# Optimization experiments

Measured on AMD Instinct MI355X. Metric: run time of the kernel, lower is better.

Reference implementation:

```python
import jax, jax.numpy as jnp
import numpy as np

B, Hh, Ww, D = 16, 32, 32, 1024
NH, HD = 16, 64
S = Hh * Ww


def _rotate_pairwise(x):
    # (..., d) -> pairwise rotation: (x0,x1,x2,x3,...) -> (-x1,x0,-x3,x2,...)
    x = x.reshape(*x.shape[:-1], -1, 2)
    x1, x2 = x[..., 0], x[..., 1]
    return jnp.stack((-x2, x1), axis=-1).reshape(*x.shape[:-2], -1)


def setup_inputs() -> dict:
    key = jax.random.key(0)
    ks = jax.random.split(key, 12)
    s = 1.0 / np.sqrt(D)
    return {
        "hidden_states": jax.random.normal(ks[0], (B, Hh, Ww, D), jnp.float32),
        "cos": jax.random.uniform(ks[1], (S, HD), jnp.float32, -1.0, 1.0),
        "sin": jax.random.uniform(ks[2], (S, HD), jnp.float32, -1.0, 1.0),
        "Wq": jax.random.normal(ks[3], (D, D), jnp.float32) * s,
        "bq": jnp.zeros((D,), jnp.float32),
        "Wk": jax.random.normal(ks[4], (D, D), jnp.float32) * s,
        "bk": jnp.zeros((D,), jnp.float32),
        "Wv": jax.random.normal(ks[5], (D, D), jnp.float32) * s,
        "bv": jnp.zeros((D,), jnp.float32),
        "Wo": jax.random.normal(ks[6], (D, D), jnp.float32) * s,
        "bo": jnp.zeros((D,), jnp.float32),
    }


def reference(hidden_states, cos, sin, Wq, bq, Wk, bk, Wv, bv, Wo, bo):
    b, h, w, d = hidden_states.shape
    seq = h * w
    x = hidden_states.reshape(b, seq, d)
    # QKV projections -> (b, heads, seq, head_dim)
    def proj(W, bias):
        y = x @ W.T + bias
        return y.reshape(b, seq, NH, HD).transpose(0, 2, 1, 3)
    q, k, v = proj(Wq, bq), proj(Wk, bk), proj(Wv, bv)
    # RoPE in fp32; cos/sin (seq, head_dim) broadcast over (b, heads)
    qf = q.astype(jnp.float32)
    kf = k.astype(jnp.float32)
    q = (qf * cos + _rotate_pairwise(qf) * sin).astype(q.dtype)
    k = (kf * cos + _rotate_pairwise(kf) * sin).astype(k.dtype)
    # SDPA
    scale = HD ** -0.5
    scores = jnp.einsum("bhqd,bhkd->bhqk", q, k) * scale
    attn = jax.nn.softmax(scores, axis=-1)
    out = jnp.einsum("bhqk,bhkd->bhqd", attn, v)
    out = out.transpose(0, 2, 1, 3).reshape(b, h, w, d)
    return out @ Wo.T + bo
```

## Files before the change

kernel.cpp:

```cpp
#include <hip/hip_runtime.h>
#include <hip/hip_bf16.h>
#include <stdint.h>

#define Bb 16
#define Ss 1024
#define Dd 1024
#define NHh 16
#define HDd 64
#define Mm 16384

typedef _Float16 half8 __attribute__((ext_vector_type(8)));
typedef float f32x4 __attribute__((ext_vector_type(4)));

__device__ __forceinline__ void gload_lds16(const _Float16* g, _Float16* l) {
  auto* gp = (const __attribute__((address_space(1))) unsigned int*)(g);
  auto* lp = (__attribute__((address_space(3))) unsigned int*)(l);
  __builtin_amdgcn_global_load_lds(gp, lp, 16, 0, 0);
}

__device__ __forceinline__ float fexp2(float x) { return __builtin_amdgcn_exp2f(x); }

__global__ void cast_all(const float* __restrict__ x,
                         const float* __restrict__ wq, const float* __restrict__ wk,
                         const float* __restrict__ wv, const float* __restrict__ wo,
                         _Float16* __restrict__ xh, _Float16* __restrict__ wcat) {
  const long NX = (long)Mm * Dd / 4;
  const long NW = (long)Dd * Dd / 4;
  long c = (long)blockIdx.x * blockDim.x + threadIdx.x;
  const float* src;
  _Float16* dst;
  long o;
  if (c < NX) {
    src = x; o = c; dst = xh;
  } else {
    long cw = c - NX;
    int m = (int)(cw / NW);
    o = cw - (long)m * NW;
    src = (m == 0) ? wq : (m == 1) ? wk : (m == 2) ? wv : wo;
    dst = wcat + (long)m * (Dd * Dd);
  }
  float4 v = reinterpret_cast<const float4*>(src)[o];
  _Float16 h[4] = {(_Float16)v.x, (_Float16)v.y, (_Float16)v.z, (_Float16)v.w};
  reinterpret_cast<uint64_t*>(dst)[o] = *reinterpret_cast<uint64_t*>(h);
}

template <int EPI>
__global__ __launch_bounds__(256, 2) void gemm_nt(
    const _Float16* __restrict__ A, const _Float16* __restrict__ Bm,
    _Float16* __restrict__ qo, _Float16* __restrict__ ko, _Float16* __restrict__ vo,
    const float* __restrict__ bq, const float* __restrict__ bk, const float* __restrict__ bv,
    const float* __restrict__ cosp, const float* __restrict__ sinp,
    float* __restrict__ outp, const float* __restrict__ bo) {
  __shared__ __align__(16) _Float16 As[128 * 32];
  __shared__ __align__(16) _Float16 Bs[128 * 32];
  const int t = threadIdx.x;
  const int w = t >> 6, l = t & 63;
  const int g = l >> 4, ln = l & 15;
  const int wr = w >> 1, wc = w & 1;
  const long rowbase = (long)blockIdx.y * 128;
  const long colbase = (long)blockIdx.x * 128;
  const _Float16* Arow0 = A + rowbase * Dd;
  const _Float16* Brow0 = Bm + colbase * Dd;

  f32x4 acc[4][4];
#pragma unroll
  for (int i = 0; i < 4; ++i)
#pragma unroll
    for (int j = 0; j < 4; ++j) acc[i][j] = f32x4{0.f, 0.f, 0.f, 0.f};

  for (int kt = 0; kt < 32; ++kt) {
    const int kof = kt * 32;
#pragma unroll
    for (int h = 0; h < 2; ++h) {
      int chunk = t + h * 256;
      int r = chunk >> 2;
      int cc = (chunk & 3) * 8;
      gload_lds16(Arow0 + (long)r * Dd + kof + cc, &As[chunk * 8]);
      gload_lds16(Brow0 + (long)r * Dd + kof + cc, &Bs[chunk * 8]);
    }
    __syncthreads();
    half8 af[4], bf[4];
#pragma unroll
    for (int i = 0; i < 4; ++i) {
      af[i] = *reinterpret_cast<const half8*>(&As[(wr * 64 + i * 16 + ln) * 32 + g * 8]);
      bf[i] = *reinterpret_cast<const half8*>(&Bs[(wc * 64 + i * 16 + ln) * 32 + g * 8]);
    }
#pragma unroll
    for (int i = 0; i < 4; ++i)
#pragma unroll
      for (int j = 0; j < 4; ++j)
        acc[i][j] = __builtin_amdgcn_mfma_f32_16x16x32_f16(af[i], bf[j], acc[i][j], 0, 0, 0);
    __syncthreads();
  }

  if (EPI == 0) {
#pragma unroll
    for (int j = 0; j < 4; ++j) {
      long n = colbase + wc * 64 + j * 16 + ln;
      int mat = (int)(n >> 10);
      int col = (int)(n & 1023);
      int hh = col >> 6, hd = col & 63;
      float bias = (mat == 0) ? bq[col] : (mat == 1) ? bk[col] : bv[col];
      if (mat < 2) {
        _Float16* dst = (mat == 0) ? qo : ko;
#pragma unroll
        for (int i = 0; i < 4; ++i) {
#pragma unroll
          for (int r = 0; r < 4; ++r) {
            long row = rowbase + wr * 64 + i * 16 + g * 4 + r;
            int b = (int)(row >> 10), s = (int)(row & 1023);
            float val = acc[i][j][r] + bias;
            float part = __shfl_xor(val, 1);
            float cv = cosp[s * HDd + hd];
            float sv = sinp[s * HDd + hd];
            val = val * cv + ((hd & 1) ? part : -part) * sv;
            dst[((long)(b * NHh + hh) * Ss + s) * HDd + hd] = (_Float16)val;
          }
        }
      } else {
#pragma unroll
        for (int i = 0; i < 4; ++i) {
          long row0 = rowbase + wr * 64 + i * 16 + g * 4;
          int b = (int)(row0 >> 10), s = (int)(row0 & 1023);
          _Float16 p4[4];
#pragma unroll
          for (int r = 0; r < 4; ++r) p4[r] = (_Float16)(acc[i][j][r] + bias);
          long addr = ((long)((b * NHh + hh) * HDd + hd)) * Ss + s;
          *reinterpret_cast<uint64_t*>(&vo[addr]) = *reinterpret_cast<uint64_t*>(p4);
        }
      }
    }
  } else {
#pragma unroll
    for (int j = 0; j < 4; ++j) {
      long n = colbase + wc * 64 + j * 16 + ln;
      float bias = bo[n];
#pragma unroll
      for (int i = 0; i < 4; ++i)
#pragma unroll
        for (int r = 0; r < 4; ++r) {
          long row = rowbase + wr * 64 + i * 16 + g * 4 + r;
          outp[row * Dd + n] = acc[i][j][r] + bias;
        }
    }
  }
}

__global__ __launch_bounds__(256, 2) void attn(
    const _Float16* __restrict__ Q, const _Float16* __restrict__ K,
    const _Float16* __restrict__ Vt_g, _Float16* __restrict__ O) {
  __shared__ __align__(16) _Float16 Ks[64 * 72];
  __shared__ __align__(16) _Float16 Vt[64 * 72];
  __shared__ __align__(16) _Float16 Ps[4 * 16 * 72];
  const int t = threadIdx.x;
  const int w = t >> 6, l = t & 63;
  const int g = l >> 4, ln = l & 15;
  const int pair = blockIdx.y;
  const int qbase = blockIdx.x * 64;
  const long pbase = (long)pair * Ss * HDd;
  const float scale2 = 0.125f * 1.44269504088896f;

  half8 qf[2];
  {
    long qr = qbase + w * 16 + ln;
    const _Float16* qp = Q + pbase + qr * HDd + g * 8;
    qf[0] = *reinterpret_cast<const half8*>(qp);
    qf[1] = *reinterpret_cast<const half8*>(qp + 32);
  }

  float m_i = -1e30f, l_i = 0.0f;
  f32x4 acc_o[4];
#pragma unroll
  for (int c = 0; c < 4; ++c) acc_o[c] = f32x4{0.f, 0.f, 0.f, 0.f};

  for (int kt = 0; kt < 16; ++kt) {
#pragma unroll
    for (int h2 = 0; h2 < 2; ++h2) {
      int chunk = t + h2 * 256;
      int r = chunk >> 3;
      int cc = (chunk & 7) * 8;
      const _Float16* kp = K + pbase + (long)(kt * 64 + r) * HDd + cc;
      *reinterpret_cast<half8*>(&Ks[r * 72 + cc]) = *reinterpret_cast<const half8*>(kp);
      const _Float16* vp = Vt_g + pbase + (long)r * Ss + kt * 64 + cc;
      *reinterpret_cast<half8*>(&Vt[r * 72 + cc]) = *reinterpret_cast<const half8*>(vp);
    }
    __syncthreads();

    f32x4 accs[4];
#pragma unroll
    for (int c = 0; c < 4; ++c) {
      half8 kf0 = *reinterpret_cast<const half8*>(&Ks[(c * 16 + ln) * 72 + g * 8]);
      half8 kf1 = *reinterpret_cast<const half8*>(&Ks[(c * 16 + ln) * 72 + 32 + g * 8]);
      f32x4 a = f32x4{0.f, 0.f, 0.f, 0.f};
      a = __builtin_amdgcn_mfma_f32_16x16x32_f16(kf0, qf[0], a, 0, 0, 0);
      a = __builtin_amdgcn_mfma_f32_16x16x32_f16(kf1, qf[1], a, 0, 0, 0);
      accs[c] = a;
    }

    float pv[16];
    float pmax = -1e30f;
#pragma unroll
    for (int c = 0; c < 4; ++c)
#pragma unroll
      for (int r = 0; r < 4; ++r) {
        float sv = accs[c][r] * scale2;
        pv[c * 4 + r] = sv;
        pmax = fmaxf(pmax, sv);
      }
    pmax = fmaxf(pmax, __shfl_xor(pmax, 16));
    pmax = fmaxf(pmax, __shfl_xor(pmax, 32));
    float m_new = fmaxf(m_i, pmax);
    float alpha = fexp2(m_i - m_new);
    float tsum = 0.0f;
#pragma unroll
    for (int z = 0; z < 16; ++z) {
      float e = fexp2(pv[z] - m_new);
      pv[z] = e;
      tsum += e;
    }
    tsum += __shfl_xor(tsum, 16);
    tsum += __shfl_xor(tsum, 32);
    l_i = l_i * alpha + tsum;
    m_i = m_new;

    float alr[4];
#pragma unroll
    for (int r = 0; r < 4; ++r) alr[r] = __shfl(alpha, g * 4 + r);
#pragma unroll
    for (int c = 0; c < 4; ++c)
#pragma unroll
      for (int r = 0; r < 4; ++r) acc_o[c][r] *= alr[r];

    _Float16* prow = &Ps[(w * 16 + ln) * 72];
#pragma unroll
    for (int c = 0; c < 4; ++c) {
      _Float16 p4[4] = {(_Float16)pv[c * 4 + 0], (_Float16)pv[c * 4 + 1],
                        (_Float16)pv[c * 4 + 2], (_Float16)pv[c * 4 + 3]};
      *reinterpret_cast<uint2*>(&prow[c * 16 + g * 4]) = *reinterpret_cast<uint2*>(p4);
    }

#pragma unroll
    for (int kh = 0; kh < 2; ++kh) {
      half8 pf = *reinterpret_cast<const half8*>(&Ps[(w * 16 + ln) * 72 + kh * 32 + g * 8]);
#pragma unroll
      for (int c = 0; c < 4; ++c) {
        half8 vf = *reinterpret_cast<const half8*>(&Vt[(c * 16 + ln) * 72 + kh * 32 + g * 8]);
        acc_o[c] = __builtin_amdgcn_mfma_f32_16x16x32_f16(pf, vf, acc_o[c], 0, 0, 0);
      }
    }
    __syncthreads();
  }

  const int b = pair >> 4, hh = pair & 15;
  float linv[4];
#pragma unroll
  for (int r = 0; r < 4; ++r) linv[r] = 1.0f / __shfl(l_i, g * 4 + r);
#pragma unroll
  for (int c = 0; c < 4; ++c)
#pragma unroll
    for (int r = 0; r < 4; ++r) {
      int s = qbase + w * 16 + g * 4 + r;
      long addr = ((long)(b * Ss + s)) * Dd + hh * HDd + c * 16 + ln;
      O[addr] = (_Float16)(acc_o[c][r] * linv[r]);
    }
}

extern "C" void kernel_launch(void* const* d_in, const int* in_sizes, int n_in,
                              void* d_out, int out_size, void* d_ws, size_t ws_size,
                              hipStream_t stream) {
  (void)in_sizes; (void)n_in; (void)out_size; (void)ws_size;
  const float* x    = (const float*)d_in[0];
  const float* cosp = (const float*)d_in[1];
  const float* sinp = (const float*)d_in[2];
  const float* Wq   = (const float*)d_in[3];
  const float* bq   = (const float*)d_in[4];
  const float* Wk   = (const float*)d_in[5];
  const float* bk   = (const float*)d_in[6];
  const float* Wv   = (const float*)d_in[7];
  const float* bv   = (const float*)d_in[8];
  const float* Wo   = (const float*)d_in[9];
  const float* bo   = (const float*)d_in[10];
  float* out = (float*)d_out;

  char* ws = (char*)d_ws;
  _Float16* xh   = (_Float16*)(ws);
  _Float16* wcat = (_Float16*)(ws + 33554432);
  _Float16* Qb   = (_Float16*)(ws + 41943040);
  _Float16* Kb   = (_Float16*)(ws + 75497472);
  _Float16* Vb   = (_Float16*)(ws + 109051904);

  cast_all<<<dim3(20480), dim3(256), 0, stream>>>(x, Wq, Wk, Wv, Wo, xh, wcat);

  gemm_nt<0><<<dim3(24, 128), dim3(256), 0, stream>>>(
      xh, wcat, Qb, Kb, Vb, bq, bk, bv, cosp, sinp, (float*)nullptr, (const float*)nullptr);

  attn<<<dim3(16, 256), dim3(256), 0, stream>>>(Qb, Kb, Vb, xh);

  gemm_nt<1><<<dim3(8, 128), dim3(256), 0, stream>>>(
      xh, wcat + (long)3072 * 1024, (_Float16*)nullptr, (_Float16*)nullptr, (_Float16*)nullptr,
      (const float*)nullptr, (const float*)nullptr, (const float*)nullptr,
      (const float*)nullptr, (const float*)nullptr, out, bo);
}
```

Before: 501.0 us.

## Prefetch next K/V tile into registers and remap attention blocks per XCD

The attention kernel now loads the next K and V tile from global memory into registers while computing on the current tile, and writes them to shared memory after the trailing barrier. This is meant to hide global load latency behind the MFMA and softmax work. The grid is also flattened to 1D, with block IDs remapped so that all 16 query tiles of a head pair land on the same XCD, which should improve L2 reuse of that pair's K/V. The cost is extra registers for the prefetch buffers, which may reduce occupancy.

New measurement: 481.3 us. -3.9%, faster.

```diff
diff --git a/kernel.cpp b/kernel.cpp
--- a/kernel.cpp
+++ b/kernel.cpp
@@ -155,10 +155,15 @@
   const int t = threadIdx.x;
   const int w = t >> 6, l = t & 63;
   const int g = l >> 4, ln = l & 15;
-  const int pair = blockIdx.y;
-  const int qbase = blockIdx.x * 64;
+  const int id = blockIdx.x;
+  const int xcd = id & 7, idx = id >> 3;
+  const int pair = xcd + 8 * (idx >> 4);
+  const int qbase = (idx & 15) * 64;
   const long pbase = (long)pair * Ss * HDd;
   const float scale2 = 0.125f * 1.44269504088896f;
+
+  const int r0 = t >> 3, cc0 = (t & 7) * 8;
+  const int r1 = (t + 256) >> 3, cc1 = cc0;
 
   half8 qf[2];
   {
@@ -173,18 +178,26 @@
 #pragma unroll
   for (int c = 0; c < 4; ++c) acc_o[c] = f32x4{0.f, 0.f, 0.f, 0.f};
 
+  half8 kreg0, kreg1, vreg0, vreg1;
+  kreg0 = *reinterpret_cast<const half8*>(K + pbase + (long)r0 * HDd + cc0);
+  kreg1 = *reinterpret_cast<const half8*>(K + pbase + (long)r1 * HDd + cc1);
+  vreg0 = *reinterpret_cast<const half8*>(Vt_g + pbase + (long)r0 * Ss + cc0);
+  vreg1 = *reinterpret_cast<const half8*>(Vt_g + pbase + (long)r1 * Ss + cc1);
+  *reinterpret_cast<half8*>(&Ks[r0 * 72 + cc0]) = kreg0;
+  *reinterpret_cast<half8*>(&Ks[r1 * 72 + cc1]) = kreg1;
+  *reinterpret_cast<half8*>(&Vt[r0 * 72 + cc0]) = vreg0;
+  *reinterpret_cast<half8*>(&Vt[r1 * 72 + cc1]) = vreg1;
+
   for (int kt = 0; kt < 16; ++kt) {
-#pragma unroll
-    for (int h2 = 0; h2 < 2; ++h2) {
-      int chunk = t + h2 * 256;
-      int r = chunk >> 3;
-      int cc = (chunk & 7) * 8;
-      const _Float16* kp = K + pbase + (long)(kt * 64 + r) * HDd + cc;
-      *reinterpret_cast<half8*>(&Ks[r * 72 + cc]) = *reinterpret_cast<const half8*>(kp);
-      const _Float16* vp = Vt_g + pbase + (long)r * Ss + kt * 64 + cc;
-      *reinterpret_cast<half8*>(&Vt[r * 72 + cc]) = *reinterpret_cast<const half8*>(vp);
-    }
     __syncthreads();
+
+    if (kt + 1 < 16) {
+      const int kb = (kt + 1) * 64;
+      kreg0 = *reinterpret_cast<const half8*>(K + pbase + (long)(kb + r0) * HDd + cc0);
+      kreg1 = *reinterpret_cast<const half8*>(K + pbase + (long)(kb + r1) * HDd + cc1);
+      vreg0 = *reinterpret_cast<const half8*>(Vt_g + pbase + (long)r0 * Ss + kb + cc0);
+      vreg1 = *reinterpret_cast<const half8*>(Vt_g + pbase + (long)r1 * Ss + kb + cc1);
+    }
 
     f32x4 accs[4];
 #pragma unroll
@@ -249,6 +262,13 @@
       }
     }
     __syncthreads();
+
+    if (kt + 1 < 16) {
+      *reinterpret_cast<half8*>(&Ks[r0 * 72 + cc0]) = kreg0;
+      *reinterpret_cast<half8*>(&Ks[r1 * 72 + cc1]) = kreg1;
+      *reinterpret_cast<half8*>(&Vt[r0 * 72 + cc0]) = vreg0;
+      *reinterpret_cast<half8*>(&Vt[r1 * 72 + cc1]) = vreg1;
+    }
   }
 
   const int b = pair >> 4, hh = pair & 15;
@@ -294,7 +314,7 @@
   gemm_nt<0><<<dim3(24, 128), dim3(256), 0, stream>>>(
       xh, wcat, Qb, Kb, Vb, bq, bk, bv, cosp, sinp, (float*)nullptr, (const float*)nullptr);
 
-  attn<<<dim3(16, 256), dim3(256), 0, stream>>>(Qb, Kb, Vb, xh);
+  attn<<<dim3(4096), dim3(256), 0, stream>>>(Qb, Kb, Vb, xh);
 
   gemm_nt<1><<<dim3(8, 128), dim3(256), 0, stream>>>(
       xh, wcat + (long)3072 * 1024, (_Float16*)nullptr, (_Float16*)nullptr, (_Float16*)nullptr,
```
